# Kernel optimization log

Hardware: AMD Instinct MI355X
Metric: run time of the kernel (lower is better)

## Reference

```python
import jax, jax.numpy as jnp
import numpy as np

EMBED_DIM = 512
NUM_HEADS = 8
WINDOW = 5
OVERLAP = 1
STRIDE = WINDOW - OVERLAP  # 4


def setup_inputs() -> dict:
    key = jax.random.key(0)
    ks = jax.random.split(key, 5)
    B, S, D = 8, 4096, EMBED_DIM
    s = 1.0 / np.sqrt(D).astype(np.float32)
    return {
        "x": jax.random.normal(ks[0], (B, S, D), jnp.float32),
        "Wq": jax.random.normal(ks[1], (D, D), jnp.float32) * s,
        "bq": jnp.zeros((D,), jnp.float32),
        "Wk": jax.random.normal(ks[2], (D, D), jnp.float32) * s,
        "bk": jnp.zeros((D,), jnp.float32),
        "Wv": jax.random.normal(ks[3], (D, D), jnp.float32) * s,
        "bv": jnp.zeros((D,), jnp.float32),
        "Wo": jax.random.normal(ks[4], (D, D), jnp.float32) * s,
        "bo": jnp.zeros((D,), jnp.float32),
    }


def reference(x, Wq, bq, Wk, bk, Wv, bv, Wo, bo):
    B, S, D = x.shape
    H = NUM_HEADS
    hd = D // H
    pad = (WINDOW - S % WINDOW) % WINDOW
    xp = jnp.pad(x, ((0, 0), (0, pad), (0, 0)))
    P = S + pad
    nw = (P - WINDOW) // STRIDE + 1

    # gather all sliding windows at once: [B, nw, W, D]
    idx = (jnp.arange(nw) * STRIDE)[:, None] + jnp.arange(WINDOW)  # [nw, W]
    win = xp[:, idx]

    def proj(t, W, b):
        return (t @ W + b).reshape(B, nw, WINDOW, H, hd)

    q = proj(win, Wq, bq)
    k = proj(win, Wk, bk)
    v = proj(win, Wv, bv)

    scale = jnp.float32(1.0 / np.sqrt(hd))
    scores = jnp.einsum('bnqhd,bnkhd->bnhqk', q, k) * scale  # [B,nw,H,W,W]
    attn = jax.nn.softmax(scores, axis=-1)
    o = jnp.einsum('bnhqk,bnkhd->bnqhd', attn, v).reshape(B, nw, WINDOW, D)
    o = o @ Wo + bo  # window outputs [B,nw,W,D]

    # overlap-add + count-average (exactly as the torch loop does)
    flat_idx = idx.reshape(-1)
    out = jnp.zeros((B, P, D), jnp.float32).at[:, flat_idx].add(
        o.reshape(B, nw * WINDOW, D))
    counts = jnp.zeros((P,), jnp.float32).at[flat_idx].add(1.0)
    out = out / (counts[None, :, None] + 1e-6)
    out = out[:, :S]

    # torch: sum(all_weights) / num_windows  -> mean over window axis
    attn_weights = attn.mean(axis=1)  # [B, H, W, W]
    return out, attn_weights
```

## Files before the change

kernel.cpp:

```cpp
#include <hip/hip_runtime.h>
#include <hip/hip_bf16.h>


#define SEQ   4096
#define NB    8
#define DIM   512
#define NWIN  1024
#define MTOT  (NB*SEQ)

typedef __bf16 bf16x8 __attribute__((ext_vector_type(8)));
typedef float  f32x4  __attribute__((ext_vector_type(4)));

__device__ __forceinline__ float b2f(unsigned short u) {
  union { unsigned int i; float f; } z; z.i = ((unsigned int)u) << 16; return z.f;
}
__device__ __forceinline__ unsigned short f2b(float f) {
  __bf16 h = (__bf16)f; return __builtin_bit_cast(unsigned short, h);
}
__device__ __forceinline__ void gload_lds16(const void* g, void* l) {
  __builtin_amdgcn_global_load_lds(
      (__attribute__((address_space(1))) void*)g,
      (__attribute__((address_space(3))) void*)l, 16, 0, 0);
}

#define FENCE() asm volatile("" ::: "memory")
#define BAR()   __builtin_amdgcn_s_barrier()
#define LGK0()  asm volatile("s_waitcnt lgkmcnt(0)" ::: "memory")
#define VMW4()  asm volatile("s_waitcnt vmcnt(4)" ::: "memory")
#define VMW0()  asm volatile("s_waitcnt vmcnt(0)" ::: "memory")

__global__ __launch_bounds__(256) void cvt_fused(
    const float* __restrict__ x, const float* __restrict__ W0,
    const float* __restrict__ W1, const float* __restrict__ W2,
    const float* __restrict__ W3,
    unsigned short* __restrict__ xb, unsigned short* __restrict__ Wt) {
  if (blockIdx.x < 2048) {
    const int n8 = MTOT * DIM / 8;
    const int stride = 2048 * 256;
    for (int i = blockIdx.x * 256 + threadIdx.x; i < n8; i += stride) {
      const float4 a = *(const float4*)(x + (size_t)i * 8);
      const float4 c = *(const float4*)(x + (size_t)i * 8 + 4);
      unsigned short u[8] = {f2b(a.x), f2b(a.y), f2b(a.z), f2b(a.w),
                             f2b(c.x), f2b(c.y), f2b(c.z), f2b(c.w)};
      *(int4*)(xb + (size_t)i * 8) = *(const int4*)u;
    }
  } else {
    __shared__ float tile[64][65];
    const int bb = blockIdx.x - 2048;
    const int w = bb >> 6;
    const int tr = (bb & 63) >> 3, tc = bb & 7;
    const float* W = (w == 0) ? W0 : (w == 1) ? W1 : (w == 2) ? W2 : W3;
    const int c = threadIdx.x & 63, r4 = threadIdx.x >> 6;
#pragma unroll
    for (int i = 0; i < 16; ++i) {
      int r = r4 + i * 4;
      tile[r][c] = W[(size_t)(tr * 64 + r) * 512 + tc * 64 + c];
    }
    __syncthreads();
    const int kk = threadIdx.x & 63, n4 = threadIdx.x >> 6;
#pragma unroll
    for (int i = 0; i < 16; ++i) {
      int nn = n4 + i * 4;
      Wt[((size_t)w << 18) + (size_t)(tc * 64 + nn) * 512 + tr * 64 + kk] =
          f2b(tile[kk][nn]);
    }
  }
}

__device__ __forceinline__ void stage_part(int h, const unsigned short* pa, const unsigned short* pb,
    int r0s, int c0s, int r1s, int c1s, char* ldsb, int wid) {
  int kt = h >> 2, slot = (h + 2) & 3;
  int buf = kt & 1, ab = slot >> 1, half = slot & 1;
  const unsigned short* src = ab ? pb : pa;
  int rb = half << 7;
  int kc = kt << 6;
  char* d = ldsb + buf * 65536 + ab * 32768 + half * 16384 + wid * 1024;
  gload_lds16(src + (size_t)(rb + r0s) * 512 + kc + c0s, d);
  gload_lds16(src + (size_t)(rb + r1s) * 512 + kc + c1s, d + 8192);
}

#define LDSB(off) (*(const bf16x8*)(ldsb + (off)))

#define RA4(BUF, HALF) { \
  _Pragma("unroll") for (int mf2 = 0; mf2 < 4; ++mf2) { \
    _Pragma("unroll") for (int ks = 0; ks < 2; ++ks) \
      a[mf2][ks] = LDSB(aS[BUF][ks] + (HALF) * 8192 + mf2 * 2048); } }

#define RB2(BUF, QN) { \
  _Pragma("unroll") for (int nf2 = 0; nf2 < 2; ++nf2) { \
    _Pragma("unroll") for (int ks = 0; ks < 2; ++ks) \
      b[(QN)*2+nf2][ks] = LDSB(bS[BUF][ks] + (QN) * 4096 + nf2 * 2048); } }

#define MMQ(QM, QN) { \
  _Pragma("unroll") for (int ks = 0; ks < 2; ++ks) \
  _Pragma("unroll") for (int mf2 = 0; mf2 < 4; ++mf2) \
  _Pragma("unroll") for (int nf2 = 0; nf2 < 2; ++nf2) \
    acc[(QM)*4+mf2][(QN)*2+nf2] = __builtin_amdgcn_mfma_f32_16x16x32_bf16( \
      a[mf2][ks], b[(QN)*2+nf2][ks], acc[(QM)*4+mf2][(QN)*2+nf2], 0, 0, 0); }

template<int MODE>
__global__ __launch_bounds__(512, 2) void gemm8(
    const unsigned short* __restrict__ A, const unsigned short* __restrict__ Bw,
    const float* __restrict__ b0, const float* __restrict__ b1, const float* __restrict__ b2,
    unsigned short* __restrict__ o0, unsigned short* __restrict__ o1, unsigned short* __restrict__ o2,
    float* __restrict__ fout,
    const float* __restrict__ abuf, float* __restrict__ aout) {
  __shared__ unsigned short lds_[65536];
  char* ldsb = (char*)lds_;

  if constexpr (MODE == 1) {
    if (blockIdx.x >= 256) {
      if (threadIdx.x < 256) {
        float* sm = (float*)lds_;
        int bh = blockIdx.x - 256;
        int b = bh >> 3, h = bh & 7;
        int t = threadIdx.x;
        float loc[25];
#pragma unroll
        for (int j = 0; j < 25; ++j) loc[j] = 0.f;
        for (int n = t; n < NWIN; n += 256) {
          const float* p = abuf + ((size_t)(b * NWIN + n) * 8 + h) * 25;
#pragma unroll
          for (int j = 0; j < 25; ++j) loc[j] += p[j];
        }
#pragma unroll
        for (int j = 0; j < 25; ++j) sm[t * 25 + j] = loc[j];
        __syncthreads();
        for (int off = 128; off > 0; off >>= 1) {
          if (t < off)
#pragma unroll
            for (int j = 0; j < 25; ++j) sm[t * 25 + j] += sm[(t + off) * 25 + j];
          __syncthreads();
        }
        if (t < 25) aout[bh * 25 + t] = sm[t] * (1.0f / 1024.0f);
      }
      return;
    }
  }

  constexpr int nwg = (MODE == 0) ? 768 : 256;
  constexpr int cpx = nwg >> 3;
  const int g = blockIdx.x;
  const int sw = (g & 7) * cpx + (g >> 3);
  constexpr int NTN = (MODE == 0) ? 6 : 2;
  const int ntile = sw % NTN, mtile = sw / NTN;
  const int m0 = mtile * 256, n0g = ntile * 256;

  const int tid = threadIdx.x;
  const int lane = tid & 63;
  const int wid = tid >> 6;
  const int wr = wid >> 2, wc = wid & 3;
  const int cl16 = lane & 15, hi = lane >> 4;
  const int hi16 = hi * 16;
  const int sxor = (cl16 & 14) << 3;

  int o0_ = tid * 16;
  int o1_ = 8192 + tid * 16;
  int l0 = o0_ ^ (((o0_ >> 8) & 7) << 4);
  int l1 = o1_ ^ (((o1_ >> 8) & 7) << 4);
  const int r0s = l0 >> 7, c0s = (l0 & 127) >> 1;
  const int r1s = l1 >> 7, c1s = (l1 & 127) >> 1;

  const unsigned short* pa = A + (size_t)m0 * 512;
  const unsigned short* pb = Bw + (size_t)n0g * 512;

  int aS[2][2], bS[2][2];
#pragma unroll
  for (int bu = 0; bu < 2; ++bu)
#pragma unroll
    for (int ks = 0; ks < 2; ++ks) {
      aS[bu][ks] = bu * 65536 + ((wr * 16384 + cl16 * 128 + ks * 64 + hi16) ^ sxor);
      bS[bu][ks] = bu * 65536 + 32768 + (((wc >> 1) * 16384 + (wc & 1) * 8192 + cl16 * 128 + ks * 64 + hi16) ^ sxor);
    }

  f32x4 acc[8][4] = {};
  bf16x8 a[4][2], b[4][2];

#define STG(H) stage_part((H), pa, pb, r0s, c0s, r1s, c1s, ldsb, wid)

  STG(0); STG(1); STG(2); STG(3); STG(4); STG(5);
  VMW4();
  FENCE(); BAR();

#pragma unroll
  for (int it = 0; it < 4; ++it) {
    const int hb = 8 * it;
    RA4(0, 0); RB2(0, 0);
    STG(hb + 6);
    FENCE(); BAR();
    __builtin_amdgcn_s_setprio(1); MMQ(0, 0); __builtin_amdgcn_s_setprio(0);
    FENCE(); BAR();
    RB2(0, 1);
    if (hb + 7 < 32) STG(hb + 7);
    FENCE(); BAR();
    __builtin_amdgcn_s_setprio(1); MMQ(0, 1); __builtin_amdgcn_s_setprio(0);
    FENCE(); BAR();
    RA4(0, 1);
    if (it < 3) STG(hb + 8);
    FENCE(); BAR();
    __builtin_amdgcn_s_setprio(1); MMQ(1, 1); __builtin_amdgcn_s_setprio(0);
    FENCE(); BAR();
    if (it < 3) STG(hb + 9);
    FENCE(); BAR();
    __builtin_amdgcn_s_setprio(1); MMQ(1, 0); __builtin_amdgcn_s_setprio(0);
    if (it < 3) { VMW4(); } else { VMW0(); }
    FENCE(); BAR();
    RA4(1, 0); RB2(1, 0);
    if (it < 3) STG(hb + 10);
    FENCE(); BAR();
    __builtin_amdgcn_s_setprio(1); MMQ(0, 0); __builtin_amdgcn_s_setprio(0);
    FENCE(); BAR();
    RB2(1, 1);
    if (it < 3) STG(hb + 11);
    FENCE(); BAR();
    __builtin_amdgcn_s_setprio(1); MMQ(0, 1); __builtin_amdgcn_s_setprio(0);
    FENCE(); BAR();
    RA4(1, 1);
    if (it < 3) STG(hb + 12);
    FENCE(); BAR();
    __builtin_amdgcn_s_setprio(1); MMQ(1, 1); __builtin_amdgcn_s_setprio(0);
    FENCE(); BAR();
    if (it < 3) STG(hb + 13);
    FENCE(); BAR();
    __builtin_amdgcn_s_setprio(1); MMQ(1, 0); __builtin_amdgcn_s_setprio(0);
    if (it < 3) { VMW4(); }
    FENCE(); BAR();
  }

  if constexpr (MODE == 0) {
    const int sel = n0g >> 9;
    const float* bias = (sel == 0) ? b0 : (sel == 1) ? b1 : b2;
    unsigned short* C = (sel == 0) ? o0 : (sel == 1) ? o1 : o2;
    const int lcb = (n0g & 511) + wc * 64;
    unsigned short* wlds = lds_ + wid * 8192;
#pragma unroll
    for (int mf = 0; mf < 8; ++mf)
#pragma unroll
      for (int nf = 0; nf < 4; ++nf) {
        float bv_ = bias[lcb + nf * 16 + cl16];
#pragma unroll
        for (int r = 0; r < 4; ++r) {
          int w = (mf * 16 + hi * 4 + r) * 64 + nf * 16 + cl16;
          wlds[w ^ (((w >> 7) & 7) << 3)] = f2b(acc[mf][nf][r] + bv_);
        }
      }
    LGK0();
#pragma unroll
    for (int itr = 0; itr < 16; ++itr) {
      int f = itr * 512 + lane * 8;
      int row = f >> 6, col = f & 63;
      int4 v = *(const int4*)&wlds[f ^ (((f >> 7) & 7) << 3)];
      *(int4*)(C + (size_t)(m0 + wr * 128 + row) * 512 + lcb + col) = v;
    }
  } else {
#pragma unroll
    for (int nf = 0; nf < 4; ++nf) {
      int ncol = n0g + wc * 64 + nf * 16 + cl16;
      float bv_ = b0[ncol];
#pragma unroll
      for (int mf = 0; mf < 8; ++mf) {
        int rbase = m0 + wr * 128 + mf * 16 + hi * 4;
#pragma unroll
        for (int r = 0; r < 4; ++r) {
          int row = rbase + r;
          int s = row & (SEQ - 1);
          float cnt = ((s & 3) == 0 && s > 0) ? 2.0f : 1.0f;
          fout[(size_t)row * 512 + ncol] = (acc[mf][nf][r] + cnt * bv_) / (cnt + 1e-6f);
        }
      }
    }
  }
}

__global__ __launch_bounds__(256) void attn_win(
    const unsigned short* __restrict__ Qb, const unsigned short* __restrict__ Kb,
    const unsigned short* __restrict__ Vb,
    const float* __restrict__ bq, const float* __restrict__ bk, const float* __restrict__ bv,
    unsigned short* __restrict__ yb, float* __restrict__ abuf) {
  const int g = blockIdx.x;
  const int swg = (g & 7) * 256 + (g >> 3);
  const int gw = swg * 4 + (threadIdx.x >> 6);
  const int b = gw >> 10, n = gw & (NWIN - 1);
  const int lane = threadIdx.x & 63;
  const int h = lane >> 3, e = lane & 7;
  const int dbase = h * 64 + e * 8;
  const size_t rowbase = (size_t)b * SEQ;

  float o4[8];
#pragma unroll
  for (int d = 0; d < 8; ++d) o4[d] = 0.f;
  if (n > 0) {
    float q0[8];
    {
      int4 qv = *(const int4*)(Qb + (rowbase + 4 * n) * DIM + dbase);
      const unsigned short* qp = (const unsigned short*)&qv;
#pragma unroll
      for (int d = 0; d < 8; ++d) q0[d] = b2f(qp[d]);
    }
    float sc[5];
#pragma unroll
    for (int j = 0; j < 5; ++j) {
      int p = 4 * n - 4 + j;
      int4 kv = *(const int4*)(Kb + (rowbase + p) * DIM + dbase);
      const unsigned short* kp = (const unsigned short*)&kv;
      float t = 0.f;
#pragma unroll
      for (int d = 0; d < 8; ++d) t += q0[d] * b2f(kp[d]);
      t += __shfl_xor(t, 1);
      t += __shfl_xor(t, 2);
      t += __shfl_xor(t, 4);
      sc[j] = t * 0.125f;
    }
    float mx = sc[0];
#pragma unroll
    for (int j = 1; j < 5; ++j) mx = fmaxf(mx, sc[j]);
    float ex[5], sum = 0.f;
#pragma unroll
    for (int j = 0; j < 5; ++j) { ex[j] = __expf(sc[j] - mx); sum += ex[j]; }
    float inv = 1.0f / sum;
#pragma unroll
    for (int j = 0; j < 5; ++j) {
      int p = 4 * n - 4 + j;
      int4 vv = *(const int4*)(Vb + (rowbase + p) * DIM + dbase);
      const unsigned short* vp = (const unsigned short*)&vv;
      float wj = ex[j] * inv;
#pragma unroll
      for (int d = 0; d < 8; ++d) o4[d] += wj * b2f(vp[d]);
    }
  }

  float kf[5][8], vf[5][8];
#pragma unroll
  for (int j = 0; j < 5; ++j) {
    int p = 4 * n + j;
    if (p < SEQ) {
      int4 kv = *(const int4*)(Kb + (rowbase + p) * DIM + dbase);
      int4 vv = *(const int4*)(Vb + (rowbase + p) * DIM + dbase);
      const unsigned short* kp = (const unsigned short*)&kv;
      const unsigned short* vp = (const unsigned short*)&vv;
#pragma unroll
      for (int d = 0; d < 8; ++d) { kf[j][d] = b2f(kp[d]); vf[j][d] = b2f(vp[d]); }
    } else {
#pragma unroll
      for (int d = 0; d < 8; ++d) { kf[j][d] = bk[dbase + d]; vf[j][d] = bv[dbase + d]; }
    }
  }
  float pm[5][5];
#pragma unroll
  for (int i = 0; i < 5; ++i) {
    int p = 4 * n + i;
    float qf[8];
    if (p < SEQ) {
      int4 qv = *(const int4*)(Qb + (rowbase + p) * DIM + dbase);
      const unsigned short* qp = (const unsigned short*)&qv;
#pragma unroll
      for (int d = 0; d < 8; ++d) qf[d] = b2f(qp[d]);
    } else {
#pragma unroll
      for (int d = 0; d < 8; ++d) qf[d] = bq[dbase + d];
    }
    float sr[5];
#pragma unroll
    for (int j = 0; j < 5; ++j) {
      float t = 0.f;
#pragma unroll
      for (int d = 0; d < 8; ++d) t += qf[d] * kf[j][d];
      t += __shfl_xor(t, 1);
      t += __shfl_xor(t, 2);
      t += __shfl_xor(t, 4);
      sr[j] = t * 0.125f;
    }
    float mx = sr[0];
#pragma unroll
    for (int j = 1; j < 5; ++j) mx = fmaxf(mx, sr[j]);
    float ex[5], sum = 0.f;
#pragma unroll
    for (int j = 0; j < 5; ++j) { ex[j] = __expf(sr[j] - mx); sum += ex[j]; }
    float inv = 1.0f / sum;
#pragma unroll
    for (int j = 0; j < 5; ++j) pm[i][j] = ex[j] * inv;
    if (i < 4) {
      float o[8];
#pragma unroll
      for (int d = 0; d < 8; ++d) o[d] = (i == 0) ? o4[d] : 0.f;
#pragma unroll
      for (int j = 0; j < 5; ++j)
#pragma unroll
        for (int d = 0; d < 8; ++d) o[d] += pm[i][j] * vf[j][d];
      unsigned short u[8];
#pragma unroll
      for (int d = 0; d < 8; ++d) u[d] = f2b(o[d]);
      *(int4*)(yb + (rowbase + p) * DIM + dbase) = *(const int4*)u;
    }
  }
  float* ap = abuf + ((size_t)(b * NWIN + n) * 8 + h) * 25;
  if (e == 0) {
#pragma unroll
    for (int i2 = 0; i2 < 5; ++i2)
#pragma unroll
      for (int j2 = 0; j2 < 5; ++j2) ap[i2 * 5 + j2] = pm[i2][j2];
  }
}

extern "C" void kernel_launch(void* const* d_in, const int* in_sizes, int n_in,
                              void* d_out, int out_size, void* d_ws, size_t ws_size,
                              hipStream_t stream) {
  const float* x  = (const float*)d_in[0];
  const float* Wq = (const float*)d_in[1];
  const float* bq = (const float*)d_in[2];
  const float* Wk = (const float*)d_in[3];
  const float* bk = (const float*)d_in[4];
  const float* Wv = (const float*)d_in[5];
  const float* bv = (const float*)d_in[6];
  const float* Wo = (const float*)d_in[7];
  const float* bo = (const float*)d_in[8];
  float* out = (float*)d_out;

  char* ws = (char*)d_ws;
  unsigned short* xb   = (unsigned short*)(ws);
  unsigned short* yb   = xb;
  unsigned short* Qb   = (unsigned short*)(ws + 33554432);
  unsigned short* Kb   = (unsigned short*)(ws + 67108864);
  unsigned short* Vb   = (unsigned short*)(ws + 100663296);
  float*          abuf = (float*)(ws + 142606336);
  unsigned short* Wt   = (unsigned short*)(ws + 149159936);
  (void)ws_size; (void)in_sizes; (void)n_in; (void)out_size;

  cvt_fused<<<2304, 256, 0, stream>>>(x, Wq, Wk, Wv, Wo, xb, Wt);
  gemm8<0><<<768, 512, 0, stream>>>(xb, Wt, bq, bk, bv, Qb, Kb, Vb, nullptr,
                                    nullptr, nullptr);
  attn_win<<<2048, 256, 0, stream>>>(Qb, Kb, Vb, bq, bk, bv, yb, abuf);
  gemm8<1><<<320, 512, 0, stream>>>(yb, Wt + 3 * (DIM * DIM), bo, nullptr, nullptr,
                                    nullptr, nullptr, nullptr, out,
                                    abuf, out + (size_t)MTOT * DIM);
}
```

Before: 145.7 us.

## Replace double-buffered 8-phase GEMM pipeline with single-buffer synchronous K loop

The GEMM kernel drops its double-buffered LDS (128KB) software pipeline with interleaved staging, priority hints and partial vmcnt waits. It now uses a single 64KB buffer: each K tile is loaded, waited on fully, then computed. The epilogue is split into two halves so it fits the smaller LDS. This halves LDS use, which may allow more blocks per CU, but global load latency is no longer overlapped with MFMA work.

```diff
diff --git a/kernel.cpp b/kernel.cpp
--- a/kernel.cpp
+++ b/kernel.cpp
@@ -26,7 +26,6 @@
 #define FENCE() asm volatile("" ::: "memory")
 #define BAR()   __builtin_amdgcn_s_barrier()
 #define LGK0()  asm volatile("s_waitcnt lgkmcnt(0)" ::: "memory")
-#define VMW4()  asm volatile("s_waitcnt vmcnt(4)" ::: "memory")
 #define VMW0()  asm volatile("s_waitcnt vmcnt(0)" ::: "memory")
 
 __global__ __launch_bounds__(256) void cvt_fused(
@@ -70,26 +69,26 @@
 __device__ __forceinline__ void stage_part(int h, const unsigned short* pa, const unsigned short* pb,
     int r0s, int c0s, int r1s, int c1s, char* ldsb, int wid) {
   int kt = h >> 2, slot = (h + 2) & 3;
-  int buf = kt & 1, ab = slot >> 1, half = slot & 1;
+  int ab = slot >> 1, half = slot & 1;
   const unsigned short* src = ab ? pb : pa;
   int rb = half << 7;
   int kc = kt << 6;
-  char* d = ldsb + buf * 65536 + ab * 32768 + half * 16384 + wid * 1024;
+  char* d = ldsb + ab * 32768 + half * 16384 + wid * 1024;
   gload_lds16(src + (size_t)(rb + r0s) * 512 + kc + c0s, d);
   gload_lds16(src + (size_t)(rb + r1s) * 512 + kc + c1s, d + 8192);
 }
 
 #define LDSB(off) (*(const bf16x8*)(ldsb + (off)))
 
-#define RA4(BUF, HALF) { \
+#define RA4(HALF) { \
   _Pragma("unroll") for (int mf2 = 0; mf2 < 4; ++mf2) { \
     _Pragma("unroll") for (int ks = 0; ks < 2; ++ks) \
-      a[mf2][ks] = LDSB(aS[BUF][ks] + (HALF) * 8192 + mf2 * 2048); } }
-
-#define RB2(BUF, QN) { \
+      a[mf2][ks] = LDSB(aS[ks] + (HALF) * 8192 + mf2 * 2048); } }
+
+#define RB2(QN) { \
   _Pragma("unroll") for (int nf2 = 0; nf2 < 2; ++nf2) { \
     _Pragma("unroll") for (int ks = 0; ks < 2; ++ks) \
-      b[(QN)*2+nf2][ks] = LDSB(bS[BUF][ks] + (QN) * 4096 + nf2 * 2048); } }
+      b[(QN)*2+nf2][ks] = LDSB(bS[ks] + (QN) * 4096 + nf2 * 2048); } }
 
 #define MMQ(QM, QN) { \
   _Pragma("unroll") for (int ks = 0; ks < 2; ++ks) \
@@ -99,13 +98,13 @@
       a[mf2][ks], b[(QN)*2+nf2][ks], acc[(QM)*4+mf2][(QN)*2+nf2], 0, 0, 0); }
 
 template<int MODE>
-__global__ __launch_bounds__(512, 2) void gemm8(
+__global__ __launch_bounds__(512, 2) void gemm1b(
     const unsigned short* __restrict__ A, const unsigned short* __restrict__ Bw,
     const float* __restrict__ b0, const float* __restrict__ b1, const float* __restrict__ b2,
     unsigned short* __restrict__ o0, unsigned short* __restrict__ o1, unsigned short* __restrict__ o2,
     float* __restrict__ fout,
     const float* __restrict__ abuf, float* __restrict__ aout) {
-  __shared__ unsigned short lds_[65536];
+  __shared__ unsigned short lds_[32768];
   char* ldsb = (char*)lds_;
 
   if constexpr (MODE == 1) {
@@ -164,67 +163,32 @@
   const unsigned short* pa = A + (size_t)m0 * 512;
   const unsigned short* pb = Bw + (size_t)n0g * 512;
 
-  int aS[2][2], bS[2][2];
-#pragma unroll
-  for (int bu = 0; bu < 2; ++bu)
-#pragma unroll
-    for (int ks = 0; ks < 2; ++ks) {
-      aS[bu][ks] = bu * 65536 + ((wr * 16384 + cl16 * 128 + ks * 64 + hi16) ^ sxor);
-      bS[bu][ks] = bu * 65536 + 32768 + (((wc >> 1) * 16384 + (wc & 1) * 8192 + cl16 * 128 + ks * 64 + hi16) ^ sxor);
-    }
+  int aS[2], bS[2];
+#pragma unroll
+  for (int ks = 0; ks < 2; ++ks) {
+    aS[ks] = (wr * 16384 + cl16 * 128 + ks * 64 + hi16) ^ sxor;
+    bS[ks] = 32768 + (((wc >> 1) * 16384 + (wc & 1) * 8192 + cl16 * 128 + ks * 64 + hi16) ^ sxor);
+  }
 
   f32x4 acc[8][4] = {};
   bf16x8 a[4][2], b[4][2];
 
-#define STG(H) stage_part((H), pa, pb, r0s, c0s, r1s, c1s, ldsb, wid)
-
-  STG(0); STG(1); STG(2); STG(3); STG(4); STG(5);
-  VMW4();
-  FENCE(); BAR();
-
-#pragma unroll
-  for (int it = 0; it < 4; ++it) {
-    const int hb = 8 * it;
-    RA4(0, 0); RB2(0, 0);
-    STG(hb + 6);
-    FENCE(); BAR();
-    __builtin_amdgcn_s_setprio(1); MMQ(0, 0); __builtin_amdgcn_s_setprio(0);
-    FENCE(); BAR();
-    RB2(0, 1);
-    if (hb + 7 < 32) STG(hb + 7);
-    FENCE(); BAR();
-    __builtin_amdgcn_s_setprio(1); MMQ(0, 1); __builtin_amdgcn_s_setprio(0);
-    FENCE(); BAR();
-    RA4(0, 1);
-    if (it < 3) STG(hb + 8);
-    FENCE(); BAR();
-    __builtin_amdgcn_s_setprio(1); MMQ(1, 1); __builtin_amdgcn_s_setprio(0);
-    FENCE(); BAR();
-    if (it < 3) STG(hb + 9);
-    FENCE(); BAR();
-    __builtin_amdgcn_s_setprio(1); MMQ(1, 0); __builtin_amdgcn_s_setprio(0);
-    if (it < 3) { VMW4(); } else { VMW0(); }
-    FENCE(); BAR();
-    RA4(1, 0); RB2(1, 0);
-    if (it < 3) STG(hb + 10);
-    FENCE(); BAR();
-    __builtin_amdgcn_s_setprio(1); MMQ(0, 0); __builtin_amdgcn_s_setprio(0);
-    FENCE(); BAR();
-    RB2(1, 1);
-    if (it < 3) STG(hb + 11);
-    FENCE(); BAR();
-    __builtin_amdgcn_s_setprio(1); MMQ(0, 1); __builtin_amdgcn_s_setprio(0);
-    FENCE(); BAR();
-    RA4(1, 1);
-    if (it < 3) STG(hb + 12);
-    FENCE(); BAR();
-    __builtin_amdgcn_s_setprio(1); MMQ(1, 1); __builtin_amdgcn_s_setprio(0);
-    FENCE(); BAR();
-    if (it < 3) STG(hb + 13);
-    FENCE(); BAR();
-    __builtin_amdgcn_s_setprio(1); MMQ(1, 0); __builtin_amdgcn_s_setprio(0);
-    if (it < 3) { VMW4(); }
-    FENCE(); BAR();
+#define STG4(KT) { stage_part((KT)*4,   pa, pb, r0s, c0s, r1s, c1s, ldsb, wid); \
+                   stage_part((KT)*4+1, pa, pb, r0s, c0s, r1s, c1s, ldsb, wid); \
+                   stage_part((KT)*4+2, pa, pb, r0s, c0s, r1s, c1s, ldsb, wid); \
+                   stage_part((KT)*4+3, pa, pb, r0s, c0s, r1s, c1s, ldsb, wid); }
+
+#pragma unroll
+  for (int kt = 0; kt < 8; ++kt) {
+    STG4(kt);
+    VMW0();
+    FENCE(); BAR(); FENCE();
+    RB2(0); RB2(1);
+    RA4(0);
+    MMQ(0, 0); MMQ(0, 1);
+    RA4(1);
+    MMQ(1, 1); MMQ(1, 0);
+    FENCE(); BAR(); FENCE();
   }
 
   if constexpr (MODE == 0) {
@@ -232,25 +196,29 @@
     const float* bias = (sel == 0) ? b0 : (sel == 1) ? b1 : b2;
     unsigned short* C = (sel == 0) ? o0 : (sel == 1) ? o1 : o2;
     const int lcb = (n0g & 511) + wc * 64;
-    unsigned short* wlds = lds_ + wid * 8192;
-#pragma unroll
-    for (int mf = 0; mf < 8; ++mf)
-#pragma unroll
-      for (int nf = 0; nf < 4; ++nf) {
-        float bv_ = bias[lcb + nf * 16 + cl16];
-#pragma unroll
-        for (int r = 0; r < 4; ++r) {
-          int w = (mf * 16 + hi * 4 + r) * 64 + nf * 16 + cl16;
-          wlds[w ^ (((w >> 7) & 7) << 3)] = f2b(acc[mf][nf][r] + bv_);
+    unsigned short* wlds = lds_ + wid * 4096;
+#pragma unroll
+    for (int hf = 0; hf < 2; ++hf) {
+#pragma unroll
+      for (int mf2 = 0; mf2 < 4; ++mf2)
+#pragma unroll
+        for (int nf = 0; nf < 4; ++nf) {
+          float bv_ = bias[lcb + nf * 16 + cl16];
+#pragma unroll
+          for (int r = 0; r < 4; ++r) {
+            int w = (mf2 * 16 + hi * 4 + r) * 64 + nf * 16 + cl16;
+            wlds[w ^ (((w >> 7) & 7) << 3)] = f2b(acc[hf * 4 + mf2][nf][r] + bv_);
+          }
         }
+      LGK0();
+#pragma unroll
+      for (int itr = 0; itr < 8; ++itr) {
+        int f = itr * 512 + lane * 8;
+        int row = f >> 6, col = f & 63;
+        int4 v = *(const int4*)&wlds[f ^ (((f >> 7) & 7) << 3)];
+        *(int4*)(C + (size_t)(m0 + wr * 128 + hf * 64 + row) * 512 + lcb + col) = v;
       }
-    LGK0();
-#pragma unroll
-    for (int itr = 0; itr < 16; ++itr) {
-      int f = itr * 512 + lane * 8;
-      int row = f >> 6, col = f & 63;
-      int4 v = *(const int4*)&wlds[f ^ (((f >> 7) & 7) << 3)];
-      *(int4*)(C + (size_t)(m0 + wr * 128 + row) * 512 + lcb + col) = v;
+      LGK0();
     }
   } else {
 #pragma unroll
@@ -427,10 +395,10 @@
   (void)ws_size; (void)in_sizes; (void)n_in; (void)out_size;
 
   cvt_fused<<<2304, 256, 0, stream>>>(x, Wq, Wk, Wv, Wo, xb, Wt);
-  gemm8<0><<<768, 512, 0, stream>>>(xb, Wt, bq, bk, bv, Qb, Kb, Vb, nullptr,
-                                    nullptr, nullptr);
+  gemm1b<0><<<768, 512, 0, stream>>>(xb, Wt, bq, bk, bv, Qb, Kb, Vb, nullptr,
+                                     nullptr, nullptr);
   attn_win<<<2048, 256, 0, stream>>>(Qb, Kb, Vb, bq, bk, bv, yb, abuf);
-  gemm8<1><<<320, 512, 0, stream>>>(yb, Wt + 3 * (DIM * DIM), bo, nullptr, nullptr,
-                                    nullptr, nullptr, nullptr, out,
-                                    abuf, out + (size_t)MTOT * DIM);
-}
+  gemm1b<1><<<320, 512, 0, stream>>>(yb, Wt + 3 * (DIM * DIM), bo, nullptr, nullptr,
+                                     nullptr, nullptr, nullptr, out,
+                                     abuf, out + (size_t)MTOT * DIM);
+}
```

Result: slower. 150.3 us (+3.2%).
